# Performance work log

Hardware: AMD Instinct MI355X
Metric: run time of the kernel (lower is better)

Reference implementation:

```python
import jax, jax.numpy as jnp
import numpy as np

B, L, C = 2, 8192, 256
K, NLEV = 17, 4
HALF = K // 2


def setup_inputs() -> dict:
    key = jax.random.key(0)
    ks = jax.random.split(key, 10)
    s = 0.02
    return {
        "x": jax.random.normal(ks[0], (B, L, C), jnp.float32),
        "stem_w": jax.random.normal(ks[1], (C, C, 2), jnp.float32) * s,   # Conv1d (out,in,k)
        "stem_b": jax.random.normal(ks[2], (C,), jnp.float32) * s,
        "qkv_w": jax.random.normal(ks[3], (3 * C, C), jnp.float32) * s,
        "width_w": jax.random.normal(ks[4], (1, C), jnp.float32) * s,
        "width_b": jax.random.normal(ks[5], (1,), jnp.float32) * s,
        "out_w": jax.random.normal(ks[6], (C, C), jnp.float32) * s,
        "query": jax.random.normal(ks[7], (NLEV * C,), jnp.float32) * s,
        "film_w": jax.random.normal(ks[8], (2 * C, NLEV * C), jnp.float32) * s,
        "film_b": jax.random.normal(ks[9], (2 * C,), jnp.float32) * s,
    }


def _local_attn(h, qkv_w, width_w, width_b, out_w):
    # h: (b, l, c); 1D local windowed attention with learned sigmoid distance mask
    b, l, c = h.shape
    rel_dist = jnp.abs(jnp.arange(K, dtype=h.dtype) - HALF)  # (K,)
    max_dist = float(HALF)
    scale = c ** -0.5
    qkv = h @ qkv_w.T
    q, k, v = jnp.split(qkv, 3, axis=-1)
    width = jax.nn.sigmoid(h @ width_w.T + width_b) * max_dist + 0.5  # (b,l,1)
    k_pad = jnp.pad(k, ((0, 0), (HALF, HALF), (0, 0)))
    v_pad = jnp.pad(v, ((0, 0), (HALF, HALF), (0, 0)))
    idx = jnp.arange(l)[:, None] + jnp.arange(K)[None, :]  # (l,K) indices into padded seq
    k_win = k_pad[:, idx]  # (b,l,K,c)
    v_win = v_pad[:, idx]  # (b,l,K,c)
    scores = jnp.einsum('blc,blwc->blw', q, k_win) * scale
    soft_mask = jax.nn.sigmoid((width - rel_dist) * 5.0)  # (b,l,K)
    scores = scores - (1.0 - soft_mask) * 10000.0
    attn = jax.nn.softmax(scores, axis=-1)
    o = jnp.einsum('blw,blwc->blc', attn, v_win)
    return (o + v) @ out_w.T


def _forward(x, stem_w, stem_b, qkv_w, width_w, width_b, out_w, query, film_w, film_b):
    b, l, c = x.shape
    # stem conv: Conv1d(C, C, kernel=2, padding=1), then narrow to first l positions
    h = jnp.transpose(x, (0, 2, 1))  # (B,C,L)
    h = jax.lax.conv_general_dilated(h, stem_w, (1,), [(1, 1)],
                                     dimension_numbers=('NCH', 'OIH', 'NCH'))
    h = h[:, :, :l] + stem_b[None, :, None]
    h = jnp.transpose(h, (0, 2, 1))  # (B,L,C)
    levels = []
    for i in range(NLEV):
        h = _local_attn(h, qkv_w, width_w, width_b, out_w)
        levels.append(h)
        if i < NLEV - 1:  # avg_pool(kernel=2, stride=2)
            bl = h.shape[1]
            h = h.reshape(b, bl // 2, 2, c).mean(axis=2)
    # nearest upsample each coarser level back to L (factors are exact powers of 2)
    ups = [levels[0]]
    for lvl in levels[1:]:
        ups.append(jnp.repeat(lvl, l // lvl.shape[1], axis=1))
    concat = jnp.concatenate(ups, axis=-1)  # (B,L,NLEV*C)
    gattn = jax.nn.softmax(concat @ query, axis=-1)  # (B,L)
    global_ctx = jnp.einsum('bl,bld->bd', gattn, concat)  # (B,NLEV*C)
    film = global_ctx @ film_w.T + film_b  # (B,2C)
    scale_f, bias_f = jnp.split(film, 2, axis=-1)
    return levels[0] * (1.0 + scale_f[:, None, :]) + bias_f[:, None, :]


def reference(x, stem_w, stem_b, qkv_w, width_w, width_b, out_w, query, film_w, film_b):
    return _forward(x, stem_w, stem_b, qkv_w, width_w, width_b, out_w, query, film_w, film_b)
```

## Files before the change

kernel.cpp:

```cpp
#include <hip/hip_runtime.h>
#include <math.h>

#define L_SEQ 8192
#define B_SZ  2
#define CH    256
#define NLEV  4

typedef __attribute__((ext_vector_type(8))) short bf16x8;
typedef __attribute__((ext_vector_type(4))) float f32x4;

static __device__ __forceinline__ float sigmoidf_(float x) {
    return 1.0f / (1.0f + expf(-x));
}

static __device__ __forceinline__ float bf2f_(unsigned short u) {
    union { unsigned int ui; float f; } x;
    x.ui = ((unsigned int)u) << 16;
    return x.f;
}
static __device__ __forceinline__ unsigned short f2b_(float f) {
    union { float f; unsigned int u; } x;
    x.f = f;
    unsigned int lsb = (x.u >> 16) & 1u;
    unsigned int r = x.u + 0x7fffu + lsb;
    return (unsigned short)(r >> 16);
}
static __device__ __forceinline__ float4 ldb4_(const unsigned short* p) {
    ushort4 u = *(const ushort4*)p;
    return make_float4(bf2f_(u.x), bf2f_(u.y), bf2f_(u.z), bf2f_(u.w));
}

__global__ void prep_kernel(const float* __restrict__ x,
                            const float* __restrict__ qkv_w,
                            const float* __restrict__ out_w,
                            const float* __restrict__ stem_w,
                            unsigned short* __restrict__ x16g,
                            unsigned short* __restrict__ qw16,
                            unsigned short* __restrict__ ow16,
                            unsigned short* __restrict__ sw16)
{
    int i = blockIdx.x * 256 + threadIdx.x;
    if (i < 256) { x16g[i] = 0; return; }
    i -= 256;
    if (i < 4194304) { x16g[256 + i] = f2b_(x[i]); return; }
    i -= 4194304;
    if (i < 196608) { qw16[i] = f2b_(qkv_w[i]); return; }
    i -= 196608;
    if (i < 65536) { ow16[i] = f2b_(out_w[i]); return; }
    i -= 65536;
    {
        int k = i & 511, n = i >> 9;
        float v = (k < 256) ? stem_w[(size_t)n * 512 + k * 2]
                            : stem_w[(size_t)n * 512 + (k - 256) * 2 + 1];
        sw16[i] = f2b_(v);
    }
}

__global__ __launch_bounds__(256) void stem_gemm_bf16(
    const unsigned short* __restrict__ x16g, const unsigned short* __restrict__ W,
    unsigned short* __restrict__ outB, const float* __restrict__ bias)
{
    __shared__ unsigned short As[128 * 32];
    __shared__ unsigned short Bs[128 * 32];
    const int tid  = threadIdx.x;
    const int wave = tid >> 6;
    const int lane = tid & 63;
    const int bm = blockIdx.y * 128;
    const int bn = blockIdx.x * 128;
    const int wm = (wave & 1) * 64;
    const int wn = (wave >> 1) * 64;
    const int srow = lane >> 2;
    const int scol = (lane & 3) * 8;

    f32x4 acc[4][4] = {};

    for (int k0 = 0; k0 < 512; k0 += 32) {
        __syncthreads();
        #pragma unroll
        for (int c = 0; c < 2; ++c) {
            const int chunk = c * 4 + wave;
            const int row = bm + chunk * 16 + srow;
            const int t = row & (L_SEQ - 1);
            const unsigned short* ga;
            if (k0 < 256)
                ga = x16g + (t > 0 ? (size_t)row * 256 : 0) + k0 + scol;
            else
                ga = x16g + ((size_t)row + 1) * 256 + (k0 - 256) + scol;
            const unsigned short* gw = W + (size_t)(bn + chunk * 16 + srow) * 512 + k0 + scol;
            __builtin_amdgcn_global_load_lds(
                (const __attribute__((address_space(1))) void*)ga,
                (__attribute__((address_space(3))) void*)(As + chunk * 16 * 32),
                16, 0, 0);
            __builtin_amdgcn_global_load_lds(
                (const __attribute__((address_space(1))) void*)gw,
                (__attribute__((address_space(3))) void*)(Bs + chunk * 16 * 32),
                16, 0, 0);
        }
        __syncthreads();

        bf16x8 af[4], bf[4];
        const int fr = lane & 15;
        const int kk = (lane >> 4) * 8;
        #pragma unroll
        for (int i = 0; i < 4; ++i) {
            af[i] = *(const bf16x8*)(As + (wm + i * 16 + fr) * 32 + kk);
            bf[i] = *(const bf16x8*)(Bs + (wn + i * 16 + fr) * 32 + kk);
        }
        #pragma unroll
        for (int i = 0; i < 4; ++i)
            #pragma unroll
            for (int j = 0; j < 4; ++j)
                acc[i][j] = __builtin_amdgcn_mfma_f32_16x16x32_bf16(
                    af[i], bf[j], acc[i][j], 0, 0, 0);
    }

    const int cn = lane & 15;
    const int cr = (lane >> 4) * 4;
    #pragma unroll
    for (int i = 0; i < 4; ++i)
        #pragma unroll
        for (int r = 0; r < 4; ++r) {
            const int m = bm + wm + i * 16 + cr + r;
            #pragma unroll
            for (int j = 0; j < 4; ++j) {
                const int n = bn + wn + j * 16 + cn;
                outB[(size_t)m * CH + n] = f2b_(acc[i][j][r] + bias[n]);
            }
        }
}

__global__ __launch_bounds__(256) void gemm_bf16(
    const unsigned short* __restrict__ A, const unsigned short* __restrict__ W,
    unsigned short* __restrict__ outB, int M, int N, int Kd)
{
    __shared__ unsigned short As[128 * 32];
    __shared__ unsigned short Bs[128 * 32];
    const int tid  = threadIdx.x;
    const int wave = tid >> 6;
    const int lane = tid & 63;
    const int bm = blockIdx.y * 128;
    const int bn = blockIdx.x * 128;
    const int wm = (wave & 1) * 64;
    const int wn = (wave >> 1) * 64;
    const int srow = lane >> 2;
    const int scol = (lane & 3) * 8;

    f32x4 acc[4][4] = {};

    for (int k0 = 0; k0 < Kd; k0 += 32) {
        __syncthreads();
        #pragma unroll
        for (int c = 0; c < 2; ++c) {
            const int chunk = c * 4 + wave;
            const int row = chunk * 16 + srow;
            const unsigned short* ga = A + (size_t)(bm + row) * Kd + k0 + scol;
            const unsigned short* gw = W + (size_t)(bn + row) * Kd + k0 + scol;
            __builtin_amdgcn_global_load_lds(
                (const __attribute__((address_space(1))) void*)ga,
                (__attribute__((address_space(3))) void*)(As + chunk * 16 * 32),
                16, 0, 0);
            __builtin_amdgcn_global_load_lds(
                (const __attribute__((address_space(1))) void*)gw,
                (__attribute__((address_space(3))) void*)(Bs + chunk * 16 * 32),
                16, 0, 0);
        }
        __syncthreads();

        bf16x8 af[4], bf[4];
        const int fr = lane & 15;
        const int kk = (lane >> 4) * 8;
        #pragma unroll
        for (int i = 0; i < 4; ++i) {
            af[i] = *(const bf16x8*)(As + (wm + i * 16 + fr) * 32 + kk);
            bf[i] = *(const bf16x8*)(Bs + (wn + i * 16 + fr) * 32 + kk);
        }
        #pragma unroll
        for (int i = 0; i < 4; ++i)
            #pragma unroll
            for (int j = 0; j < 4; ++j)
                acc[i][j] = __builtin_amdgcn_mfma_f32_16x16x32_bf16(
                    af[i], bf[j], acc[i][j], 0, 0, 0);
    }

    const int cn = lane & 15;
    const int cr = (lane >> 4) * 4;
    #pragma unroll
    for (int i = 0; i < 4; ++i)
        #pragma unroll
        for (int r = 0; r < 4; ++r) {
            const int m = bm + wm + i * 16 + cr + r;
            const size_t rowoff = (size_t)m * N;
            #pragma unroll
            for (int j = 0; j < 4; ++j)
                outB[rowoff + bn + wn + j * 16 + cn] = f2b_(acc[i][j][r]);
        }
}

__global__ __launch_bounds__(256) void gemm_out_bf16(
    const unsigned short* __restrict__ A, const unsigned short* __restrict__ W,
    unsigned short* __restrict__ outB, unsigned short* __restrict__ dsB, int M)
{
    __shared__ unsigned short As[128 * 32];
    __shared__ unsigned short Bs[128 * 32];
    const int tid  = threadIdx.x;
    const int wave = tid >> 6;
    const int lane = tid & 63;
    const int bm = blockIdx.y * 128;
    const int bn = blockIdx.x * 128;
    const int wm = (wave & 1) * 64;
    const int wn = (wave >> 1) * 64;
    const int srow = lane >> 2;
    const int scol = (lane & 3) * 8;

    f32x4 acc[4][4] = {};

    for (int k0 = 0; k0 < 256; k0 += 32) {
        __syncthreads();
        #pragma unroll
        for (int c = 0; c < 2; ++c) {
            const int chunk = c * 4 + wave;
            const int row = chunk * 16 + srow;
            const unsigned short* ga = A + (size_t)(bm + row) * 256 + k0 + scol;
            const unsigned short* gw = W + (size_t)(bn + row) * 256 + k0 + scol;
            __builtin_amdgcn_global_load_lds(
                (const __attribute__((address_space(1))) void*)ga,
                (__attribute__((address_space(3))) void*)(As + chunk * 16 * 32),
                16, 0, 0);
            __builtin_amdgcn_global_load_lds(
                (const __attribute__((address_space(1))) void*)gw,
                (__attribute__((address_space(3))) void*)(Bs + chunk * 16 * 32),
                16, 0, 0);
        }
        __syncthreads();

        bf16x8 af[4], bf[4];
        const int fr = lane & 15;
        const int kk = (lane >> 4) * 8;
        #pragma unroll
        for (int i = 0; i < 4; ++i) {
            af[i] = *(const bf16x8*)(As + (wm + i * 16 + fr) * 32 + kk);
            bf[i] = *(const bf16x8*)(Bs + (wn + i * 16 + fr) * 32 + kk);
        }
        #pragma unroll
        for (int i = 0; i < 4; ++i)
            #pragma unroll
            for (int j = 0; j < 4; ++j)
                acc[i][j] = __builtin_amdgcn_mfma_f32_16x16x32_bf16(
                    af[i], bf[j], acc[i][j], 0, 0, 0);
    }

    const int cn = lane & 15;
    const int cr = (lane >> 4) * 4;
    #pragma unroll
    for (int i = 0; i < 4; ++i) {
        const int base = bm + wm + i * 16 + cr;
        #pragma unroll
        for (int j = 0; j < 4; ++j) {
            const int col = bn + wn + j * 16 + cn;
            float v0 = acc[i][j][0], v1 = acc[i][j][1];
            float v2 = acc[i][j][2], v3 = acc[i][j][3];
            outB[(size_t)(base + 0) * CH + col] = f2b_(v0);
            outB[(size_t)(base + 1) * CH + col] = f2b_(v1);
            outB[(size_t)(base + 2) * CH + col] = f2b_(v2);
            outB[(size_t)(base + 3) * CH + col] = f2b_(v3);
            if (dsB) {
                dsB[(size_t)(base >> 1) * CH + col]       = f2b_(0.5f * (v0 + v1));
                dsB[(size_t)((base >> 1) + 1) * CH + col] = f2b_(0.5f * (v2 + v3));
            }
        }
    }
}

__global__ __launch_bounds__(256) void attn_mfma_kernel(
    const unsigned short* __restrict__ qkv, const unsigned short* __restrict__ h16,
    const float* __restrict__ ww, const float* __restrict__ wbp,
    unsigned short* __restrict__ ov, int l)
{
    __shared__ unsigned short kv[22528];
    __shared__ unsigned short pb[4 * 512];

    const int tid  = threadIdx.x;
    const int wave = tid >> 6;
    const int lane = tid & 63;
    const int q    = lane >> 4;
    const int n    = lane & 15;

    const int blocks_per_seq = l >> 6;
    const int b  = blockIdx.x / blocks_per_seq;
    const int t0 = (blockIdx.x % blocks_per_seq) << 6;
    const size_t seqbase = (size_t)b * l;
    const int row0 = t0 + wave * 16;

    #pragma unroll
    for (int i = 0; i < 10; ++i) {
        int task = i * 256 + tid;
        int r = task >> 5, chunk = task & 31;
        int grow = t0 - 8 + r;
        bf16x8 val = {0, 0, 0, 0, 0, 0, 0, 0};
        if (grow >= 0 && grow < l)
            val = *(const bf16x8*)(qkv + (seqbase + grow) * 768 + 256 + chunk * 8);
        *(bf16x8*)(kv + r * 272 + chunk * 8) = val;
    }

    float wdot = 0.0f;
    {
        const unsigned short* hrow = h16 + (seqbase + row0 + n) * 256 + q * 64;
        #pragma unroll
        for (int jj = 0; jj < 8; ++jj) {
            bf16x8 hv = *(const bf16x8*)(hrow + jj * 8);
            float4 wa = *((const float4*)(ww + q * 64 + jj * 8));
            float4 wc = *((const float4*)(ww + q * 64 + jj * 8 + 4));
            wdot += bf2f_(((unsigned short*)&hv)[0]) * wa.x
                  + bf2f_(((unsigned short*)&hv)[1]) * wa.y
                  + bf2f_(((unsigned short*)&hv)[2]) * wa.z
                  + bf2f_(((unsigned short*)&hv)[3]) * wa.w
                  + bf2f_(((unsigned short*)&hv)[4]) * wc.x
                  + bf2f_(((unsigned short*)&hv)[5]) * wc.y
                  + bf2f_(((unsigned short*)&hv)[6]) * wc.z
                  + bf2f_(((unsigned short*)&hv)[7]) * wc.w;
        }
    }
    wdot += __shfl_xor(wdot, 16, 64);
    wdot += __shfl_xor(wdot, 32, 64);
    const float w_n = sigmoidf_(wdot + wbp[0]) * 8.0f + 0.5f;

    __syncthreads();

    bf16x8 qf[8];
    const unsigned short* qrow = qkv + (seqbase + row0 + n) * 768;
    #pragma unroll
    for (int kk = 0; kk < 8; ++kk)
        qf[kk] = *(const bf16x8*)(qrow + kk * 32 + q * 8);

    f32x4 accS[2] = {};
    #pragma unroll
    for (int kk = 0; kk < 8; ++kk) {
        #pragma unroll
        for (int h = 0; h < 2; ++h) {
            bf16x8 bk = *(const bf16x8*)(kv + (wave * 16 + h * 16 + n) * 272 +
                                         kk * 32 + q * 8);
            accS[h] = __builtin_amdgcn_mfma_f32_16x16x32_bf16(
                qf[kk], bk, accS[h], 0, 0, 0);
        }
    }

    float wd[4];
    #pragma unroll
    for (int r = 0; r < 4; ++r) wd[r] = __shfl(w_n, q * 4 + r, 64);

    float s[2][4];
    #pragma unroll
    for (int h = 0; h < 2; ++h)
        #pragma unroll
        for (int r = 0; r < 4; ++r) {
            int ii = q * 4 + r;
            int c  = h * 16 + n;
            int w  = c - ii;
            float dist = fabsf((float)w - 8.0f);
            float sm = sigmoidf_((wd[r] - dist) * 5.0f);
            float v = accS[h][r] * 0.0625f - (1.0f - sm) * 10000.0f;
            s[h][r] = (w >= 0 && w <= 16) ? v : -3.0e38f;
        }

    float mx[4], sum[4];
    #pragma unroll
    for (int r = 0; r < 4; ++r) mx[r] = fmaxf(s[0][r], s[1][r]);
    #pragma unroll
    for (int m = 1; m < 16; m <<= 1)
        #pragma unroll
        for (int r = 0; r < 4; ++r) mx[r] = fmaxf(mx[r], __shfl_xor(mx[r], m, 64));
    float e[2][4];
    #pragma unroll
    for (int h = 0; h < 2; ++h)
        #pragma unroll
        for (int r = 0; r < 4; ++r) e[h][r] = expf(s[h][r] - mx[r]);
    #pragma unroll
    for (int r = 0; r < 4; ++r) sum[r] = e[0][r] + e[1][r];
    #pragma unroll
    for (int m = 1; m < 16; m <<= 1)
        #pragma unroll
        for (int r = 0; r < 4; ++r) sum[r] += __shfl_xor(sum[r], m, 64);

    #pragma unroll
    for (int h = 0; h < 2; ++h)
        #pragma unroll
        for (int r = 0; r < 4; ++r) {
            int ii = q * 4 + r, c = h * 16 + n;
            float p = e[h][r] / sum[r];
            if (c == ii + 8) p += 1.0f;
            pb[wave * 512 + ii * 32 + c] = f2b_(p);
        }
    __syncthreads();

    #pragma unroll
    for (int p5 = 0; p5 < 5; ++p5)
        #pragma unroll
        for (int cc = 0; cc < 2; ++cc) {
            int r = p5 * 16 + (tid & 15);
            int chunk = cc * 16 + (tid >> 4);
            int grow = t0 - 8 + r;
            bf16x8 val = {0, 0, 0, 0, 0, 0, 0, 0};
            if (grow >= 0 && grow < l)
                val = *(const bf16x8*)(qkv + (seqbase + grow) * 768 + 512 + chunk * 8);
            #pragma unroll
            for (int jj = 0; jj < 8; ++jj)
                kv[(chunk * 8 + jj) * 88 + r] = ((unsigned short*)&val)[jj];
        }
    __syncthreads();

    bf16x8 pf = *(const bf16x8*)(pb + wave * 512 + n * 32 + q * 8);
    const size_t obase = (seqbase + row0) * 256;
    #pragma unroll
    for (int chunk = 0; chunk < 16; ++chunk) {
        bf16x8 vf = *(const bf16x8*)(kv + (chunk * 16 + n) * 88 + wave * 16 + q * 8);
        f32x4 z = {};
        f32x4 o = __builtin_amdgcn_mfma_f32_16x16x32_bf16(pf, vf, z, 0, 0, 0);
        #pragma unroll
        for (int r = 0; r < 4; ++r)
            ov[obase + (size_t)(q * 4 + r) * 256 + chunk * 16 + n] = f2b_(o[r]);
    }
}

__global__ __launch_bounds__(1024) void tail_ctx_kernel(
    const unsigned short* __restrict__ l0, const unsigned short* __restrict__ l1,
    const unsigned short* __restrict__ l2, const unsigned short* __restrict__ l3,
    const float* __restrict__ query, float* __restrict__ partials,
    float* __restrict__ denomP)
{
    __shared__ float eS[128];
    const int tid = threadIdx.x;
    const int chunk = blockIdx.x, b = blockIdx.y;
    const int t0 = chunk * 128;
    const unsigned short* levp[4] = {l0, l1, l2, l3};

    const int w = tid >> 6, lane = tid & 63;
    const int lev = lane >> 4, c0 = (lane & 15) * 16;
    const unsigned short* lpbase = levp[lev] + (size_t)b * (L_SEQ >> lev) * CH;
    const float* qp = query + lev * CH + c0;
    float4 q0 = *(const float4*)(qp);
    float4 q1 = *(const float4*)(qp + 4);
    float4 q2 = *(const float4*)(qp + 8);
    float4 q3 = *(const float4*)(qp + 12);
    #pragma unroll
    for (int j = 0; j < 8; ++j) {
        int t = t0 + w * 8 + j;
        const unsigned short* p = lpbase + (size_t)(t >> lev) * CH + c0;
        float4 h0 = ldb4_(p), h1 = ldb4_(p + 4), h2 = ldb4_(p + 8), h3 = ldb4_(p + 12);
        float part = h0.x * q0.x + h0.y * q0.y + h0.z * q0.z + h0.w * q0.w
                   + h1.x * q1.x + h1.y * q1.y + h1.z * q1.z + h1.w * q1.w
                   + h2.x * q2.x + h2.y * q2.y + h2.z * q2.z + h2.w * q2.w
                   + h3.x * q3.x + h3.y * q3.y + h3.z * q3.z + h3.w * q3.w;
        #pragma unroll
        for (int m = 1; m < 64; m <<= 1) part += __shfl_xor(part, m, 64);
        if (lane == 0) eS[w * 8 + j] = expf(part);
    }
    __syncthreads();

    if (tid == 0) {
        float ds = 0.0f;
        #pragma unroll 8
        for (int i = 0; i < 128; ++i) ds += eS[i];
        denomP[b * 64 + chunk] = ds;
    }

    const int dlev = tid >> 8, c = tid & 255;
    const unsigned short* lp = levp[dlev] + (size_t)b * (L_SEQ >> dlev) * CH;
    float acc = 0.0f;
    #pragma unroll 4
    for (int t = t0; t < t0 + 128; ++t)
        acc += eS[t - t0] * bf2f_(lp[(size_t)(t >> dlev) * CH + c]);
    partials[(size_t)(b * 64 + chunk) * 1024 + tid] = acc;
}

__global__ __launch_bounds__(256) void ctx_reduce_kernel(
    const float* __restrict__ partials, const float* __restrict__ denomP,
    float* __restrict__ ctx)
{
    const int b = blockIdx.y;
    const int d = blockIdx.x * 256 + threadIdx.x;
    float acc = 0.0f;
    #pragma unroll
    for (int c = 0; c < 64; ++c) acc += partials[(size_t)(b * 64 + c) * 1024 + d];
    float den = 0.0f;
    #pragma unroll
    for (int c = 0; c < 64; ++c) den += denomP[b * 64 + c];
    ctx[b * 1024 + d] = acc / den;
}

__global__ __launch_bounds__(256) void film_kernel(
    const float* __restrict__ ctx, const float* __restrict__ fw,
    const float* __restrict__ fb, float* __restrict__ film)
{
    const int lane = threadIdx.x & 63;
    const int j = blockIdx.x * 4 + (threadIdx.x >> 6);
    float acc0 = 0.0f, acc1 = 0.0f;
    #pragma unroll
    for (int r = 0; r < 4; ++r) {
        float4 w4 = *((const float4*)(fw + (size_t)j * 1024 + r * 256) + lane);
        float4 c0 = *((const float4*)(ctx + r * 256) + lane);
        float4 c1 = *((const float4*)(ctx + 1024 + r * 256) + lane);
        acc0 += w4.x * c0.x + w4.y * c0.y + w4.z * c0.z + w4.w * c0.w;
        acc1 += w4.x * c1.x + w4.y * c1.y + w4.z * c1.z + w4.w * c1.w;
    }
    #pragma unroll
    for (int m = 1; m < 64; m <<= 1) {
        acc0 += __shfl_xor(acc0, m, 64);
        acc1 += __shfl_xor(acc1, m, 64);
    }
    if (lane == 0) {
        float b = fb[j];
        film[j] = acc0 + b;
        film[512 + j] = acc1 + b;
    }
}

__global__ void final_kernel(const unsigned short* __restrict__ lev0,
                             const float* __restrict__ film,
                             float* __restrict__ out)
{
    size_t n4 = ((size_t)blockIdx.x * 256 + threadIdx.x) * 4;
    int c = (int)(n4 & (CH - 1));
    int b = (int)(n4 >> 21);
    float4 h = ldb4_(lev0 + n4);
    const float* fs = film + b * 512;
    float4 o;
    o.x = h.x * (1.0f + fs[c + 0]) + fs[256 + c + 0];
    o.y = h.y * (1.0f + fs[c + 1]) + fs[256 + c + 1];
    o.z = h.z * (1.0f + fs[c + 2]) + fs[256 + c + 2];
    o.w = h.w * (1.0f + fs[c + 3]) + fs[256 + c + 3];
    *(float4*)(out + n4) = o;
}

extern "C" void kernel_launch(void* const* d_in, const int* in_sizes, int n_in,
                              void* d_out, int out_size, void* d_ws, size_t ws_size,
                              hipStream_t stream) {
    const float* x       = (const float*)d_in[0];
    const float* stem_w  = (const float*)d_in[1];
    const float* stem_b  = (const float*)d_in[2];
    const float* qkv_w   = (const float*)d_in[3];
    const float* width_w = (const float*)d_in[4];
    const float* width_b = (const float*)d_in[5];
    const float* out_w   = (const float*)d_in[6];
    const float* query   = (const float*)d_in[7];
    const float* film_w  = (const float*)d_in[8];
    const float* film_b  = (const float*)d_in[9];
    float* out = (float*)d_out;
    float* ws  = (float*)d_ws;

    float* partials = ws;
    float* denomP   = partials + 131072;
    float* ctx      = denomP + 128;
    float* film     = ctx + 2048;
    unsigned short* x16g  = (unsigned short*)(film + 1024);
    unsigned short* h16_0 = x16g + 4194560;
    unsigned short* h16_1 = h16_0 + 4194304;
    unsigned short* h16_2 = h16_1 + 2097152;
    unsigned short* h16_3 = h16_2 + 1048576;
    unsigned short* qkv16 = h16_3 + 524288;
    unsigned short* ov16  = qkv16 + 12582912;
    unsigned short* l16_0 = ov16 + 4194304;
    unsigned short* l16_1 = l16_0 + 4194304;
    unsigned short* l16_2 = l16_1 + 2097152;
    unsigned short* l16_3 = l16_2 + 1048576;
    unsigned short* qw16  = l16_3 + 524288;
    unsigned short* ow16  = qw16 + 196608;
    unsigned short* sw16  = ow16 + 65536;
    unsigned short* h16[4]  = {h16_0, h16_1, h16_2, h16_3};
    unsigned short* l16[4]  = {l16_0, l16_1, l16_2, l16_3};

    prep_kernel<<<(256 + 4194304 + 196608 + 65536 + 131072) / 256, 256, 0, stream>>>(
        x, qkv_w, out_w, stem_w, x16g, qw16, ow16, sw16);

    stem_gemm_bf16<<<dim3(CH / 128, B_SZ * L_SEQ / 128), 256, 0, stream>>>(
        x16g, sw16, h16_0, stem_b);

    for (int i = 0; i < NLEV; ++i) {
        const int l = L_SEQ >> i;
        const int M = B_SZ * l;
        gemm_bf16<<<dim3(768 / 128, M / 128), 256, 0, stream>>>(
            h16[i], qw16, qkv16, M, 768, CH);
        attn_mfma_kernel<<<M / 64, 256, 0, stream>>>(
            qkv16, h16[i], width_w, width_b, ov16, l);
        gemm_out_bf16<<<dim3(CH / 128, M / 128), 256, 0, stream>>>(
            ov16, ow16, l16[i], (i < NLEV - 1) ? h16[i + 1] : nullptr, M);
    }

    tail_ctx_kernel<<<dim3(64, B_SZ), 1024, 0, stream>>>(
        l16_0, l16_1, l16_2, l16_3, query, partials, denomP);
    ctx_reduce_kernel<<<dim3(4, B_SZ), 256, 0, stream>>>(partials, denomP, ctx);
    film_kernel<<<128, 256, 0, stream>>>(ctx, film_w, film_b, film);
    final_kernel<<<(B_SZ * L_SEQ * CH) / 1024, 256, 0, stream>>>(l16_0, film, out);
}
```

Before: 266.2 us.

## Fuse output projection into local attention kernel via LDS-staged tile

The separate output-projection GEMM (which also wrote the downsampled next-level input) is folded into the attention kernel. Each 64-row attention tile stages its bf16 (o+v) result in swizzled LDS, reusing the K/V buffer, then multiplies by out_w read straight from global memory and writes both the level output and the averaged downsample. This removes the ov16 global round trip and one kernel launch per level. In exchange each block reloads the whole 256x256 out_w from global/L2 and adds extra barriers. MFMA sections are also wrapped in s_setprio hints.

```diff
diff --git a/kernel.cpp b/kernel.cpp
--- a/kernel.cpp
+++ b/kernel.cpp
@@ -196,85 +196,11 @@
         }
 }
 
-__global__ __launch_bounds__(256) void gemm_out_bf16(
-    const unsigned short* __restrict__ A, const unsigned short* __restrict__ W,
-    unsigned short* __restrict__ outB, unsigned short* __restrict__ dsB, int M)
-{
-    __shared__ unsigned short As[128 * 32];
-    __shared__ unsigned short Bs[128 * 32];
-    const int tid  = threadIdx.x;
-    const int wave = tid >> 6;
-    const int lane = tid & 63;
-    const int bm = blockIdx.y * 128;
-    const int bn = blockIdx.x * 128;
-    const int wm = (wave & 1) * 64;
-    const int wn = (wave >> 1) * 64;
-    const int srow = lane >> 2;
-    const int scol = (lane & 3) * 8;
-
-    f32x4 acc[4][4] = {};
-
-    for (int k0 = 0; k0 < 256; k0 += 32) {
-        __syncthreads();
-        #pragma unroll
-        for (int c = 0; c < 2; ++c) {
-            const int chunk = c * 4 + wave;
-            const int row = chunk * 16 + srow;
-            const unsigned short* ga = A + (size_t)(bm + row) * 256 + k0 + scol;
-            const unsigned short* gw = W + (size_t)(bn + row) * 256 + k0 + scol;
-            __builtin_amdgcn_global_load_lds(
-                (const __attribute__((address_space(1))) void*)ga,
-                (__attribute__((address_space(3))) void*)(As + chunk * 16 * 32),
-                16, 0, 0);
-            __builtin_amdgcn_global_load_lds(
-                (const __attribute__((address_space(1))) void*)gw,
-                (__attribute__((address_space(3))) void*)(Bs + chunk * 16 * 32),
-                16, 0, 0);
-        }
-        __syncthreads();
-
-        bf16x8 af[4], bf[4];
-        const int fr = lane & 15;
-        const int kk = (lane >> 4) * 8;
-        #pragma unroll
-        for (int i = 0; i < 4; ++i) {
-            af[i] = *(const bf16x8*)(As + (wm + i * 16 + fr) * 32 + kk);
-            bf[i] = *(const bf16x8*)(Bs + (wn + i * 16 + fr) * 32 + kk);
-        }
-        #pragma unroll
-        for (int i = 0; i < 4; ++i)
-            #pragma unroll
-            for (int j = 0; j < 4; ++j)
-                acc[i][j] = __builtin_amdgcn_mfma_f32_16x16x32_bf16(
-                    af[i], bf[j], acc[i][j], 0, 0, 0);
-    }
-
-    const int cn = lane & 15;
-    const int cr = (lane >> 4) * 4;
-    #pragma unroll
-    for (int i = 0; i < 4; ++i) {
-        const int base = bm + wm + i * 16 + cr;
-        #pragma unroll
-        for (int j = 0; j < 4; ++j) {
-            const int col = bn + wn + j * 16 + cn;
-            float v0 = acc[i][j][0], v1 = acc[i][j][1];
-            float v2 = acc[i][j][2], v3 = acc[i][j][3];
-            outB[(size_t)(base + 0) * CH + col] = f2b_(v0);
-            outB[(size_t)(base + 1) * CH + col] = f2b_(v1);
-            outB[(size_t)(base + 2) * CH + col] = f2b_(v2);
-            outB[(size_t)(base + 3) * CH + col] = f2b_(v3);
-            if (dsB) {
-                dsB[(size_t)(base >> 1) * CH + col]       = f2b_(0.5f * (v0 + v1));
-                dsB[(size_t)((base >> 1) + 1) * CH + col] = f2b_(0.5f * (v2 + v3));
-            }
-        }
-    }
-}
-
-__global__ __launch_bounds__(256) void attn_mfma_kernel(
+__global__ __launch_bounds__(256) void attn_fused_kernel(
     const unsigned short* __restrict__ qkv, const unsigned short* __restrict__ h16,
     const float* __restrict__ ww, const float* __restrict__ wbp,
-    unsigned short* __restrict__ ov, int l)
+    const unsigned short* __restrict__ ow,
+    unsigned short* __restrict__ l16o, unsigned short* __restrict__ dsB, int l)
 {
     __shared__ unsigned short kv[22528];
     __shared__ unsigned short pb[4 * 512];
@@ -333,6 +259,7 @@
         qf[kk] = *(const bf16x8*)(qrow + kk * 32 + q * 8);
 
     f32x4 accS[2] = {};
+    __builtin_amdgcn_s_setprio(1);
     #pragma unroll
     for (int kk = 0; kk < 8; ++kk) {
         #pragma unroll
@@ -343,6 +270,7 @@
                 qf[kk], bk, accS[h], 0, 0, 0);
         }
     }
+    __builtin_amdgcn_s_setprio(0);
 
     float wd[4];
     #pragma unroll
@@ -409,15 +337,94 @@
     __syncthreads();
 
     bf16x8 pf = *(const bf16x8*)(pb + wave * 512 + n * 32 + q * 8);
-    const size_t obase = (seqbase + row0) * 256;
-    #pragma unroll
-    for (int chunk = 0; chunk < 16; ++chunk) {
-        bf16x8 vf = *(const bf16x8*)(kv + (chunk * 16 + n) * 88 + wave * 16 + q * 8);
+    f32x4 po[8];
+    __builtin_amdgcn_s_setprio(1);
+    #pragma unroll
+    for (int c = 0; c < 8; ++c) {
+        bf16x8 vf = *(const bf16x8*)(kv + (c * 16 + n) * 88 + wave * 16 + q * 8);
         f32x4 z = {};
-        f32x4 o = __builtin_amdgcn_mfma_f32_16x16x32_bf16(pf, vf, z, 0, 0, 0);
-        #pragma unroll
-        for (int r = 0; r < 4; ++r)
-            ov[obase + (size_t)(q * 4 + r) * 256 + chunk * 16 + n] = f2b_(o[r]);
+        po[c] = __builtin_amdgcn_mfma_f32_16x16x32_bf16(pf, vf, z, 0, 0, 0);
+    }
+    __builtin_amdgcn_s_setprio(0);
+    __syncthreads();
+    {
+        char* orsB = (char*)kv;
+        #pragma unroll
+        for (int c = 0; c < 8; ++c)
+            #pragma unroll
+            for (int r = 0; r < 4; ++r) {
+                const int row = wave * 16 + q * 4 + r;
+                *(unsigned short*)(orsB +
+                    ((row * 256 + c * 32 + 2 * n) ^ ((row & 7) << 4))) = f2b_(po[c][r]);
+            }
+    }
+    __builtin_amdgcn_s_setprio(1);
+    #pragma unroll
+    for (int c = 0; c < 8; ++c) {
+        bf16x8 vf = *(const bf16x8*)(kv + ((c + 8) * 16 + n) * 88 + wave * 16 + q * 8);
+        f32x4 z = {};
+        po[c] = __builtin_amdgcn_mfma_f32_16x16x32_bf16(pf, vf, z, 0, 0, 0);
+    }
+    __builtin_amdgcn_s_setprio(0);
+    __syncthreads();
+    {
+        char* orsB = (char*)(kv + 8192);
+        #pragma unroll
+        for (int c = 0; c < 8; ++c)
+            #pragma unroll
+            for (int r = 0; r < 4; ++r) {
+                const int row = wave * 16 + q * 4 + r;
+                *(unsigned short*)(orsB +
+                    ((row * 256 + c * 32 + 2 * n) ^ ((row & 7) << 4))) = f2b_(po[c][r]);
+            }
+    }
+    __syncthreads();
+
+    f32x4 acc[4][4] = {};
+    const unsigned short* owb = ow + (size_t)(wave * 64) * 256;
+    #pragma unroll
+    for (int k0 = 0; k0 < 256; k0 += 32) {
+        const char* Ab = (const char*)(kv + ((k0 & 128) ? 8192 : 0));
+        const int kb = ((k0 & 127) + q * 8) * 2;
+        bf16x8 af[4], bv[4];
+        #pragma unroll
+        for (int i = 0; i < 4; ++i) {
+            const int row = i * 16 + n;
+            af[i] = *(const bf16x8*)(Ab + ((row * 256 + kb) ^ ((n & 7) << 4)));
+        }
+        #pragma unroll
+        for (int j = 0; j < 4; ++j)
+            bv[j] = *(const bf16x8*)(owb + (size_t)(j * 16 + n) * 256 + k0 + q * 8);
+        __builtin_amdgcn_s_setprio(1);
+        #pragma unroll
+        for (int i = 0; i < 4; ++i)
+            #pragma unroll
+            for (int j = 0; j < 4; ++j)
+                acc[i][j] = __builtin_amdgcn_mfma_f32_16x16x32_bf16(
+                    af[i], bv[j], acc[i][j], 0, 0, 0);
+        __builtin_amdgcn_s_setprio(0);
+    }
+
+    const size_t gbase = seqbase + t0;
+    #pragma unroll
+    for (int i = 0; i < 4; ++i) {
+        const int rl = i * 16 + q * 4;
+        #pragma unroll
+        for (int j = 0; j < 4; ++j) {
+            const int col = wave * 64 + j * 16 + n;
+            float v0 = acc[i][j][0], v1 = acc[i][j][1];
+            float v2 = acc[i][j][2], v3 = acc[i][j][3];
+            size_t r0 = (gbase + rl) * CH + col;
+            l16o[r0]           = f2b_(v0);
+            l16o[r0 + CH]      = f2b_(v1);
+            l16o[r0 + 2 * CH]  = f2b_(v2);
+            l16o[r0 + 3 * CH]  = f2b_(v3);
+            if (dsB) {
+                size_t d0 = ((gbase + rl) >> 1) * CH + col;
+                dsB[d0]      = f2b_(0.5f * (v0 + v1));
+                dsB[d0 + CH] = f2b_(0.5f * (v2 + v3));
+            }
+        }
     }
 }
 
@@ -567,6 +574,7 @@
     unsigned short* sw16  = ow16 + 65536;
     unsigned short* h16[4]  = {h16_0, h16_1, h16_2, h16_3};
     unsigned short* l16[4]  = {l16_0, l16_1, l16_2, l16_3};
+    (void)ov16;
 
     prep_kernel<<<(256 + 4194304 + 196608 + 65536 + 131072) / 256, 256, 0, stream>>>(
         x, qkv_w, out_w, stem_w, x16g, qw16, ow16, sw16);
@@ -579,10 +587,9 @@
         const int M = B_SZ * l;
         gemm_bf16<<<dim3(768 / 128, M / 128), 256, 0, stream>>>(
             h16[i], qw16, qkv16, M, 768, CH);
-        attn_mfma_kernel<<<M / 64, 256, 0, stream>>>(
-            qkv16, h16[i], width_w, width_b, ov16, l);
-        gemm_out_bf16<<<dim3(CH / 128, M / 128), 256, 0, stream>>>(
-            ov16, ow16, l16[i], (i < NLEV - 1) ? h16[i + 1] : nullptr, M);
+        attn_fused_kernel<<<M / 64, 256, 0, stream>>>(
+            qkv16, h16[i], width_w, width_b, ow16,
+            l16[i], (i < NLEV - 1) ? h16[i + 1] : nullptr, l);
     }
 
     tail_ctx_kernel<<<dim3(64, B_SZ), 1024, 0, stream>>>(
```

After: 257.9 us. 1.03x faster.
